# Kernel optimization log

Measured on AMD Instinct MI355X. Metric: run time of the kernel, lower is better.

Reference implementation:

```python
import jax, jax.numpy as jnp
import numpy as np

N_NODES = 100000
N_EDGES = 1600000
IN_CH = 128
OUT_CH = 64
NEG_SLOPE = 0.2
EPS = 1e-10


def setup_inputs() -> dict:
    key = jax.random.key(0)
    k1, k2, k3, k4, k5 = jax.random.split(key, 5)
    x = jax.random.normal(k1, (N_NODES, IN_CH), dtype=jnp.float32)
    edge_index = jax.random.randint(k2, (2, N_EDGES), 0, N_NODES, dtype=jnp.int64)
    W = jax.random.normal(k3, (OUT_CH, IN_CH), dtype=jnp.float32) * (1.0 / np.sqrt(IN_CH))
    a_l = jax.random.normal(k4, (OUT_CH,), dtype=jnp.float32) * (1.0 / np.sqrt(OUT_CH))
    a_r = jax.random.normal(k5, (OUT_CH,), dtype=jnp.float32) * (1.0 / np.sqrt(OUT_CH))
    bias = jnp.zeros((OUT_CH,), dtype=jnp.float32)
    return {"x": x, "edge_index": edge_index, "W": W, "a_l": a_l, "a_r": a_r, "bias": bias}


def reference(x, edge_index, W, a_l, a_r, bias):
    N = x.shape[0]
    h = x @ W.T                     # (N, out_ch)
    src, dst = edge_index[0], edge_index[1]
    e_l = h @ a_l                   # (N,)
    e_r = h @ a_r                   # (N,)
    edge_attn = jax.nn.leaky_relu(e_l[dst] + e_r[src], negative_slope=NEG_SLOPE)  # (E,)
    # segment softmax over incoming edges of each dst node
    edge_max = jax.ops.segment_max(edge_attn, dst, num_segments=N)  # (N,), -inf for isolated
    edge_attn = jnp.exp(edge_attn - edge_max[dst])
    edge_sum = jax.ops.segment_sum(edge_attn, dst, num_segments=N)  # (N,)
    edge_attn = edge_attn / (edge_sum[dst] + EPS)
    messages = h[src] * edge_attn[:, None]                          # (E, out_ch)
    out = jax.ops.segment_sum(messages, dst, num_segments=N)        # (N, out_ch)
    return out + bias
```

## Files before the change

### kernel.cpp

```cpp
#include <hip/hip_runtime.h>
#include <math.h>

#define NN 100000
#define NE 1600000
#define IC 128
#define OC 64
#define NEG_SLOPE 0.2f
#define EPS_F 1e-10f

#define NSLICE 500
#define SN 200
#define EB 500
#define QPB 800
#define CAP 3600
#define SLEN (NSLICE * EB)

typedef short bf16x8 __attribute__((ext_vector_type(8)));
typedef float f32x4 __attribute__((ext_vector_type(4)));

__device__ __forceinline__ unsigned short f2bf(float f) {
    unsigned u = __float_as_uint(f);
    u += 0x7fff + ((u >> 16) & 1);
    return (unsigned short)(u >> 16);
}

__global__ __launch_bounds__(256) void linear_kernel(
    const float* __restrict__ x, const float* __restrict__ W,
    const float* __restrict__ a_l, const float* __restrict__ a_r,
    unsigned short* __restrict__ h_bf, float* __restrict__ e_l,
    float* __restrict__ e_r)
{
    __shared__ unsigned short lds[128 * 136];
    const int tid = threadIdx.x;
    const int n0 = blockIdx.x * 64;

#pragma unroll
    for (int it = 0; it < 8; it++) {
        int i = it * 256 + tid;
        int r = i >> 5, c4 = i & 31;
        int n = n0 + r;
        float4 v = make_float4(0.f, 0.f, 0.f, 0.f);
        if (n < NN) v = *(const float4*)&x[(size_t)n * 128 + (c4 << 2)];
        ushort4 b;
        b.x = f2bf(v.x); b.y = f2bf(v.y); b.z = f2bf(v.z); b.w = f2bf(v.w);
        *(ushort4*)&lds[r * 136 + (c4 << 2)] = b;
    }
#pragma unroll
    for (int it = 0; it < 8; it++) {
        int i = it * 256 + tid;
        int r = i >> 5, c4 = i & 31;
        float4 v = *(const float4*)&W[r * 128 + (c4 << 2)];
        ushort4 b;
        b.x = f2bf(v.x); b.y = f2bf(v.y); b.z = f2bf(v.z); b.w = f2bf(v.w);
        *(ushort4*)&lds[(64 + r) * 136 + (c4 << 2)] = b;
    }
    __syncthreads();

    const int wv = tid >> 6;
    const int lane = tid & 63;
    const int q = lane >> 4;
    const int c = lane & 15;

    f32x4 acc[4];
#pragma unroll
    for (int t = 0; t < 4; t++) acc[t] = (f32x4){0.f, 0.f, 0.f, 0.f};

    const unsigned short* xrow = &lds[(wv * 16 + c) * 136];
    const unsigned short* wrow = &lds[(64 + c) * 136];

#pragma unroll
    for (int kk = 0; kk < 4; kk++) {
        int ko = kk * 32 + q * 8;
        bf16x8 a = *(const bf16x8*)&xrow[ko];
#pragma unroll
        for (int t = 0; t < 4; t++) {
            bf16x8 b = *(const bf16x8*)&wrow[t * 16 * 136 + ko];
            acc[t] = __builtin_amdgcn_mfma_f32_16x16x32_bf16(a, b, acc[t], 0, 0, 0);
        }
    }

#pragma unroll
    for (int r = 0; r < 4; r++) {
        int m = n0 + wv * 16 + q * 4 + r;
        if (m < NN) {
#pragma unroll
            for (int t = 0; t < 4; t++)
                h_bf[(size_t)m * OC + t * 16 + c] = f2bf(acc[t][r]);
        }
    }

    float al[4], ar[4];
#pragma unroll
    for (int t = 0; t < 4; t++) { al[t] = a_l[t * 16 + c]; ar[t] = a_r[t * 16 + c]; }
    float pl[4], pr[4];
#pragma unroll
    for (int r = 0; r < 4; r++) {
        pl[r] = al[0] * acc[0][r] + al[1] * acc[1][r] + al[2] * acc[2][r] + al[3] * acc[3][r];
        pr[r] = ar[0] * acc[0][r] + ar[1] * acc[1][r] + ar[2] * acc[2][r] + ar[3] * acc[3][r];
    }
#pragma unroll
    for (int m = 1; m < 16; m <<= 1) {
#pragma unroll
        for (int r = 0; r < 4; r++) {
            pl[r] += __shfl_xor(pl[r], m);
            pr[r] += __shfl_xor(pr[r], m);
        }
    }
    if (c == 0) {
#pragma unroll
        for (int r = 0; r < 4; r++) {
            int m = n0 + wv * 16 + q * 4 + r;
            if (m < NN) { e_l[m] = pl[r]; e_r[m] = pr[r]; }
        }
    }
}

__global__ __launch_bounds__(256) void hist_kernel(
    const int* __restrict__ dst, int* __restrict__ H)
{
    __shared__ int hist[NSLICE];
    const int t = threadIdx.x, b = blockIdx.x;
    for (int i = t; i < NSLICE; i += 256) hist[i] = 0;
    __syncthreads();
    for (int qi = t; qi < QPB; qi += 256) {
        int4 d = ((const int4*)dst)[b * QPB + qi];
        atomicAdd(&hist[d.x / SN], 1);
        atomicAdd(&hist[d.y / SN], 1);
        atomicAdd(&hist[d.z / SN], 1);
        atomicAdd(&hist[d.w / SN], 1);
    }
    __syncthreads();
    for (int i = t; i < NSLICE; i += 256) H[i * EB + b] = hist[i];
}

__global__ __launch_bounds__(1024) void scan_block_kernel(
    const int* __restrict__ deg, int* __restrict__ offsets,
    int* __restrict__ bsums)
{
    __shared__ int wsum[16];
    const int t = threadIdx.x;
    const int lane = t & 63, wv = t >> 6;
    const int i = blockIdx.x * 1024 + t;
    int v = (i < SLEN) ? deg[i] : 0;
    int incl = v;
#pragma unroll
    for (int off = 1; off < 64; off <<= 1) {
        int u = __shfl_up(incl, off);
        if (lane >= off) incl += u;
    }
    if (lane == 63) wsum[wv] = incl;
    __syncthreads();
    if (wv == 0 && lane < 16) {
        int s = wsum[lane];
        int si = s;
#pragma unroll
        for (int off = 1; off < 16; off <<= 1) {
            int u = __shfl_up(si, off);
            if (lane >= off) si += u;
        }
        wsum[lane] = si - s;
    }
    __syncthreads();
    int excl = incl - v + wsum[wv];
    if (i < SLEN) offsets[i] = excl;
    if (t == 1023) bsums[blockIdx.x] = excl + v;
}

__global__ __launch_bounds__(256) void scan_bsums_kernel(int* __restrict__ bsums)
{
    __shared__ int s[256];
    const int t = threadIdx.x;
    const int NB = (SLEN + 1023) / 1024;
    int v = (t < NB) ? bsums[t] : 0;
    s[t] = v;
    __syncthreads();
    for (int off = 1; off < 256; off <<= 1) {
        int u = (t >= off) ? s[t - off] : 0;
        __syncthreads();
        s[t] += u;
        __syncthreads();
    }
    if (t < NB) bsums[t] = s[t] - v;
}

__global__ __launch_bounds__(256) void bucket_kernel(
    const int* __restrict__ src, const int* __restrict__ dst,
    const int* __restrict__ O_raw, const int* __restrict__ bsums,
    int* __restrict__ bucketed)
{
    __shared__ int cur[NSLICE];
    const int t = threadIdx.x, b = blockIdx.x;
    for (int i = t; i < NSLICE; i += 256) {
        int gi = i * EB + b;
        cur[i] = O_raw[gi] + bsums[gi >> 10];
    }
    __syncthreads();
    for (int qi = t; qi < QPB; qi += 256) {
        int4 d4 = ((const int4*)dst)[b * QPB + qi];
        int4 s4 = ((const int4*)src)[b * QPB + qi];
        int dd[4] = {d4.x, d4.y, d4.z, d4.w};
        int ss[4] = {s4.x, s4.y, s4.z, s4.w};
#pragma unroll
        for (int k = 0; k < 4; k++) {
            int sl = dd[k] / SN;
            int pos = atomicAdd(&cur[sl], 1);
            bucketed[pos] = ((dd[k] - sl * SN) << 17) | ss[k];
        }
    }
}

__global__ __launch_bounds__(1024, 8) void fused_sort_agg_kernel(
    const int* __restrict__ bucketed, const int* __restrict__ O_raw,
    const int* __restrict__ bsums, const float* __restrict__ e_l,
    const float* __restrict__ e_r, const unsigned short* __restrict__ h_bf,
    const float* __restrict__ bias, float* __restrict__ out)
{
    __shared__ int2 sorted[CAP];
    __shared__ int hist[SN];
    __shared__ float el[SN];
    __shared__ int wsums[4];

    const int s = blockIdx.x, t = threadIdx.x;
    int gi0 = s * EB;
    const int B0 = O_raw[gi0] + bsums[gi0 >> 10];
    int B1 = NE;
    if (s < NSLICE - 1) {
        int gi1 = (s + 1) * EB;
        B1 = O_raw[gi1] + bsums[gi1 >> 10];
    }
    int cnt = B1 - B0;
    if (cnt > CAP) cnt = CAP;

    if (t < SN) {
        hist[t] = 0;
        el[t] = e_l[s * SN + t];
    }
    __syncthreads();

    int pr[4]; float wr[4];
#pragma unroll
    for (int k = 0; k < 4; k++) {
        int i = t + k * 1024;
        if (i < cnt) {
            int p = __builtin_nontemporal_load(&bucketed[B0 + i]);
            int dloc = p >> 17;
            float a = el[dloc] + e_r[p & 0x1FFFF];
            a = (a > 0.f) ? a : NEG_SLOPE * a;
            float w = __expf(a);
            pr[k] = p; wr[k] = w;
            atomicAdd(&hist[dloc], 1);
        }
    }
    __syncthreads();

    const int lane = t & 63, w4 = t >> 6;
    int v = (t < SN) ? hist[t] : 0;
    int incl = v;
#pragma unroll
    for (int o = 1; o < 64; o <<= 1) {
        int u = __shfl_up(incl, o);
        if (lane >= o) incl += u;
    }
    if (w4 < 4 && lane == 63) wsums[w4] = incl;
    __syncthreads();
    if (t == 0) {
        int run = 0;
#pragma unroll
        for (int k = 0; k < 4; k++) { int x = wsums[k]; wsums[k] = run; run += x; }
    }
    __syncthreads();
    int excl = incl - v + ((w4 < 4) ? wsums[w4] : 0);
    if (t < SN) hist[t] = excl;
    __syncthreads();

#pragma unroll
    for (int k = 0; k < 4; k++) {
        int i = t + k * 1024;
        if (i < cnt) {
            int dloc = pr[k] >> 17;
            int pos = atomicAdd(&hist[dloc], 1);
            sorted[pos] = make_int2(pr[k] & 0x1FFFF, __float_as_int(wr[k]));
        }
    }
    __syncthreads();

    const int g = t >> 3;
    const int ch = (t & 7) * 8;
    float4 bb0 = *(const float4*)&bias[ch];
    float4 bb1 = *(const float4*)&bias[ch + 4];

    for (int n = g; n < SN; n += 128) {
        const int start = (n == 0) ? 0 : hist[n - 1];
        const int end = hist[n];
        float acc[8] = {0.f, 0.f, 0.f, 0.f, 0.f, 0.f, 0.f, 0.f};
        float ws = 0.f;

        for (int j = start; j < end; j += 4) {
#pragma unroll
            for (int u = 0; u < 4; u++) {
                int e = j + u;
                int ec = (e < end) ? e : (end - 1);
                int2 p = sorted[ec];
                float w = (e < end) ? __int_as_float(p.y) : 0.f;
                const unsigned short* hp = h_bf + (((unsigned)p.x << 6) + ch);
                uint4 qv = *(const uint4*)hp;
                ws += w;
                acc[0] += w * __uint_as_float(qv.x << 16);
                acc[1] += w * __uint_as_float(qv.x & 0xffff0000u);
                acc[2] += w * __uint_as_float(qv.y << 16);
                acc[3] += w * __uint_as_float(qv.y & 0xffff0000u);
                acc[4] += w * __uint_as_float(qv.z << 16);
                acc[5] += w * __uint_as_float(qv.z & 0xffff0000u);
                acc[6] += w * __uint_as_float(qv.w << 16);
                acc[7] += w * __uint_as_float(qv.w & 0xffff0000u);
            }
        }

        float rinv = 1.0f / (ws + EPS_F);
        int node = s * SN + n;
        f32x4 o0 = { acc[0] * rinv + bb0.x, acc[1] * rinv + bb0.y,
                     acc[2] * rinv + bb0.z, acc[3] * rinv + bb0.w };
        f32x4 o1 = { acc[4] * rinv + bb1.x, acc[5] * rinv + bb1.y,
                     acc[6] * rinv + bb1.z, acc[7] * rinv + bb1.w };
        __builtin_nontemporal_store(o0, (f32x4*)&out[(size_t)node * OC + ch]);
        __builtin_nontemporal_store(o1, (f32x4*)&out[(size_t)node * OC + ch + 4]);
    }
}

extern "C" void kernel_launch(void* const* d_in, const int* in_sizes, int n_in,
                              void* d_out, int out_size, void* d_ws, size_t ws_size,
                              hipStream_t stream)
{
    const float* x = (const float*)d_in[0];
    const int* edge_index = (const int*)d_in[1];
    const float* W = (const float*)d_in[2];
    const float* a_l = (const float*)d_in[3];
    const float* a_r = (const float*)d_in[4];
    const float* bias = (const float*)d_in[5];
    float* out = (float*)d_out;

    const int* src = edge_index;
    const int* dst = edge_index + NE;

    char* w = (char*)d_ws;
    unsigned short* h_bf = (unsigned short*)w;
    size_t off = (size_t)NN * OC * 2;
    float* e_l = (float*)(w + off); off += (size_t)NN * 4;
    float* e_r = (float*)(w + off); off += (size_t)NN * 4;
    int* H = (int*)(w + off);       off += (size_t)SLEN * 4;
    int* O_raw = (int*)(w + off);   off += (size_t)(SLEN + 4) * 4;
    int* bsums = (int*)(w + off);   off += 256 * 4;
    int* bucketed = (int*)(w + off); off += (size_t)NE * 4;

    linear_kernel<<<(NN + 63) / 64, 256, 0, stream>>>(x, W, a_l, a_r, h_bf, e_l, e_r);
    hist_kernel<<<EB, 256, 0, stream>>>(dst, H);
    scan_block_kernel<<<(SLEN + 1023) / 1024, 1024, 0, stream>>>(H, O_raw, bsums);
    scan_bsums_kernel<<<1, 256, 0, stream>>>(bsums);
    bucket_kernel<<<EB, 256, 0, stream>>>(src, dst, O_raw, bsums, bucketed);
    fused_sort_agg_kernel<<<NSLICE, 1024, 0, stream>>>(bucketed, O_raw, bsums, e_l, e_r,
                                                       h_bf, bias, out);
}
```

Baseline: 175.4 us.

## Replace global scan-based bucketing with fixed-capacity slice segments and atomic cursors

```diff
diff --git a/kernel.cpp b/kernel.cpp
--- a/kernel.cpp
+++ b/kernel.cpp
@@ -12,8 +12,8 @@
 #define SN 200
 #define EB 500
 #define QPB 800
-#define CAP 3600
-#define SLEN (NSLICE * EB)
+#define EPB 3200
+#define CAPSEG 3600
 
 typedef short bf16x8 __attribute__((ext_vector_type(8)));
 typedef float f32x4 __attribute__((ext_vector_type(4)));
@@ -28,11 +28,15 @@
     const float* __restrict__ x, const float* __restrict__ W,
     const float* __restrict__ a_l, const float* __restrict__ a_r,
     unsigned short* __restrict__ h_bf, float* __restrict__ e_l,
-    float* __restrict__ e_r)
+    float* __restrict__ e_r, int* __restrict__ gcur)
 {
     __shared__ unsigned short lds[128 * 136];
     const int tid = threadIdx.x;
     const int n0 = blockIdx.x * 64;
+
+    if (blockIdx.x == 0) {
+        for (int i = tid; i < NSLICE; i += 256) gcur[i] = 0;
+    }
 
 #pragma unroll
     for (int it = 0; it < 8; it++) {
@@ -115,13 +119,21 @@
     }
 }
 
-__global__ __launch_bounds__(256) void hist_kernel(
-    const int* __restrict__ dst, int* __restrict__ H)
+__global__ __launch_bounds__(256) void bucket2_kernel(
+    const int* __restrict__ src, const int* __restrict__ dst,
+    int* __restrict__ gcur, int* __restrict__ bucketed)
 {
     __shared__ int hist[NSLICE];
+    __shared__ int base[NSLICE];
+    __shared__ int lcur[NSLICE];
+    __shared__ int gp[EPB];
+    __shared__ int pay[EPB];
+    __shared__ int wsums[4];
+
     const int t = threadIdx.x, b = blockIdx.x;
     for (int i = t; i < NSLICE; i += 256) hist[i] = 0;
     __syncthreads();
+
     for (int qi = t; qi < QPB; qi += 256) {
         int4 d = ((const int4*)dst)[b * QPB + qi];
         atomicAdd(&hist[d.x / SN], 1);
@@ -130,71 +142,40 @@
         atomicAdd(&hist[d.w / SN], 1);
     }
     __syncthreads();
-    for (int i = t; i < NSLICE; i += 256) H[i * EB + b] = hist[i];
-}
-
-__global__ __launch_bounds__(1024) void scan_block_kernel(
-    const int* __restrict__ deg, int* __restrict__ offsets,
-    int* __restrict__ bsums)
-{
-    __shared__ int wsum[16];
-    const int t = threadIdx.x;
-    const int lane = t & 63, wv = t >> 6;
-    const int i = blockIdx.x * 1024 + t;
-    int v = (i < SLEN) ? deg[i] : 0;
-    int incl = v;
-#pragma unroll
-    for (int off = 1; off < 64; off <<= 1) {
-        int u = __shfl_up(incl, off);
-        if (lane >= off) incl += u;
-    }
-    if (lane == 63) wsum[wv] = incl;
-    __syncthreads();
-    if (wv == 0 && lane < 16) {
-        int s = wsum[lane];
-        int si = s;
-#pragma unroll
-        for (int off = 1; off < 16; off <<= 1) {
-            int u = __shfl_up(si, off);
-            if (lane >= off) si += u;
-        }
-        wsum[lane] = si - s;
-    }
-    __syncthreads();
-    int excl = incl - v + wsum[wv];
-    if (i < SLEN) offsets[i] = excl;
-    if (t == 1023) bsums[blockIdx.x] = excl + v;
-}
-
-__global__ __launch_bounds__(256) void scan_bsums_kernel(int* __restrict__ bsums)
-{
-    __shared__ int s[256];
-    const int t = threadIdx.x;
-    const int NB = (SLEN + 1023) / 1024;
-    int v = (t < NB) ? bsums[t] : 0;
-    s[t] = v;
-    __syncthreads();
-    for (int off = 1; off < 256; off <<= 1) {
-        int u = (t >= off) ? s[t - off] : 0;
-        __syncthreads();
-        s[t] += u;
-        __syncthreads();
-    }
-    if (t < NB) bsums[t] = s[t] - v;
-}
-
-__global__ __launch_bounds__(256) void bucket_kernel(
-    const int* __restrict__ src, const int* __restrict__ dst,
-    const int* __restrict__ O_raw, const int* __restrict__ bsums,
-    int* __restrict__ bucketed)
-{
-    __shared__ int cur[NSLICE];
-    const int t = threadIdx.x, b = blockIdx.x;
-    for (int i = t; i < NSLICE; i += 256) {
-        int gi = i * EB + b;
-        cur[i] = O_raw[gi] + bsums[gi >> 10];
-    }
-    __syncthreads();
+
+    const int lane = t & 63, w4 = t >> 6;
+    int a0 = (2 * t < NSLICE) ? hist[2 * t] : 0;
+    int a1 = (2 * t + 1 < NSLICE) ? hist[2 * t + 1] : 0;
+    int pairsum = a0 + a1;
+    int incl = pairsum;
+#pragma unroll
+    for (int o = 1; o < 64; o <<= 1) {
+        int u = __shfl_up(incl, o);
+        if (lane >= o) incl += u;
+    }
+    if (lane == 63) wsums[w4] = incl;
+    __syncthreads();
+    if (t == 0) {
+        int run = 0;
+#pragma unroll
+        for (int k = 0; k < 4; k++) { int x = wsums[k]; wsums[k] = run; run += x; }
+    }
+    __syncthreads();
+    int excl = incl - pairsum + wsums[w4];
+    if (2 * t < NSLICE) {
+        int s0 = 2 * t;
+        base[s0] = s0 * CAPSEG + atomicAdd(&gcur[s0], a0);
+        hist[s0] = excl;
+        lcur[s0] = excl;
+    }
+    if (2 * t + 1 < NSLICE) {
+        int s1 = 2 * t + 1;
+        base[s1] = s1 * CAPSEG + atomicAdd(&gcur[s1], a1);
+        hist[s1] = excl + a0;
+        lcur[s1] = excl + a0;
+    }
+    __syncthreads();
+
     for (int qi = t; qi < QPB; qi += 256) {
         int4 d4 = ((const int4*)dst)[b * QPB + qi];
         int4 s4 = ((const int4*)src)[b * QPB + qi];
@@ -203,33 +184,36 @@
 #pragma unroll
         for (int k = 0; k < 4; k++) {
             int sl = dd[k] / SN;
-            int pos = atomicAdd(&cur[sl], 1);
-            bucketed[pos] = ((dd[k] - sl * SN) << 17) | ss[k];
-        }
+            int slot = atomicAdd(&lcur[sl], 1);
+            int gpos = base[sl] + (slot - hist[sl]);
+            if (gpos - sl * CAPSEG >= CAPSEG) gpos = -1;
+            gp[slot] = gpos;
+            pay[slot] = ((dd[k] - sl * SN) << 17) | ss[k];
+        }
+    }
+    __syncthreads();
+
+    for (int i = t; i < EPB; i += 256) {
+        int gpos = gp[i];
+        if (gpos >= 0) bucketed[gpos] = pay[i];
     }
 }
 
 __global__ __launch_bounds__(1024, 8) void fused_sort_agg_kernel(
-    const int* __restrict__ bucketed, const int* __restrict__ O_raw,
-    const int* __restrict__ bsums, const float* __restrict__ e_l,
-    const float* __restrict__ e_r, const unsigned short* __restrict__ h_bf,
-    const float* __restrict__ bias, float* __restrict__ out)
+    const int* __restrict__ bucketed, const int* __restrict__ gcur,
+    const float* __restrict__ e_l, const float* __restrict__ e_r,
+    const unsigned short* __restrict__ h_bf, const float* __restrict__ bias,
+    float* __restrict__ out)
 {
-    __shared__ int2 sorted[CAP];
+    __shared__ int2 sorted[CAPSEG];
     __shared__ int hist[SN];
     __shared__ float el[SN];
     __shared__ int wsums[4];
 
     const int s = blockIdx.x, t = threadIdx.x;
-    int gi0 = s * EB;
-    const int B0 = O_raw[gi0] + bsums[gi0 >> 10];
-    int B1 = NE;
-    if (s < NSLICE - 1) {
-        int gi1 = (s + 1) * EB;
-        B1 = O_raw[gi1] + bsums[gi1 >> 10];
-    }
-    int cnt = B1 - B0;
-    if (cnt > CAP) cnt = CAP;
+    const int B0 = s * CAPSEG;
+    int cnt = gcur[s];
+    if (cnt > CAPSEG) cnt = CAPSEG;
 
     if (t < SN) {
         hist[t] = 0;
@@ -296,23 +280,28 @@
         float ws = 0.f;
 
         for (int j = start; j < end; j += 4) {
+            int2 pp[4];
 #pragma unroll
             for (int u = 0; u < 4; u++) {
                 int e = j + u;
-                int ec = (e < end) ? e : (end - 1);
-                int2 p = sorted[ec];
-                float w = (e < end) ? __int_as_float(p.y) : 0.f;
-                const unsigned short* hp = h_bf + (((unsigned)p.x << 6) + ch);
-                uint4 qv = *(const uint4*)hp;
+                pp[u] = sorted[(e < end) ? e : (end - 1)];
+            }
+            uint4 qq[4];
+#pragma unroll
+            for (int u = 0; u < 4; u++)
+                qq[u] = *(const uint4*)(h_bf + (((unsigned)pp[u].x << 6) + ch));
+#pragma unroll
+            for (int u = 0; u < 4; u++) {
+                float w = (j + u < end) ? __int_as_float(pp[u].y) : 0.f;
                 ws += w;
-                acc[0] += w * __uint_as_float(qv.x << 16);
-                acc[1] += w * __uint_as_float(qv.x & 0xffff0000u);
-                acc[2] += w * __uint_as_float(qv.y << 16);
-                acc[3] += w * __uint_as_float(qv.y & 0xffff0000u);
-                acc[4] += w * __uint_as_float(qv.z << 16);
-                acc[5] += w * __uint_as_float(qv.z & 0xffff0000u);
-                acc[6] += w * __uint_as_float(qv.w << 16);
-                acc[7] += w * __uint_as_float(qv.w & 0xffff0000u);
+                acc[0] += w * __uint_as_float(qq[u].x << 16);
+                acc[1] += w * __uint_as_float(qq[u].x & 0xffff0000u);
+                acc[2] += w * __uint_as_float(qq[u].y << 16);
+                acc[3] += w * __uint_as_float(qq[u].y & 0xffff0000u);
+                acc[4] += w * __uint_as_float(qq[u].z << 16);
+                acc[5] += w * __uint_as_float(qq[u].z & 0xffff0000u);
+                acc[6] += w * __uint_as_float(qq[u].w << 16);
+                acc[7] += w * __uint_as_float(qq[u].w & 0xffff0000u);
             }
         }
 
@@ -347,16 +336,11 @@
     size_t off = (size_t)NN * OC * 2;
     float* e_l = (float*)(w + off); off += (size_t)NN * 4;
     float* e_r = (float*)(w + off); off += (size_t)NN * 4;
-    int* H = (int*)(w + off);       off += (size_t)SLEN * 4;
-    int* O_raw = (int*)(w + off);   off += (size_t)(SLEN + 4) * 4;
-    int* bsums = (int*)(w + off);   off += 256 * 4;
-    int* bucketed = (int*)(w + off); off += (size_t)NE * 4;
-
-    linear_kernel<<<(NN + 63) / 64, 256, 0, stream>>>(x, W, a_l, a_r, h_bf, e_l, e_r);
-    hist_kernel<<<EB, 256, 0, stream>>>(dst, H);
-    scan_block_kernel<<<(SLEN + 1023) / 1024, 1024, 0, stream>>>(H, O_raw, bsums);
-    scan_bsums_kernel<<<1, 256, 0, stream>>>(bsums);
-    bucket_kernel<<<EB, 256, 0, stream>>>(src, dst, O_raw, bsums, bucketed);
-    fused_sort_agg_kernel<<<NSLICE, 1024, 0, stream>>>(bucketed, O_raw, bsums, e_l, e_r,
+    int* gcur = (int*)(w + off);    off += (size_t)512 * 4;
+    int* bucketed = (int*)(w + off); off += (size_t)NSLICE * CAPSEG * 4;
+
+    linear_kernel<<<(NN + 63) / 64, 256, 0, stream>>>(x, W, a_l, a_r, h_bf, e_l, e_r, gcur);
+    bucket2_kernel<<<EB, 256, 0, stream>>>(src, dst, gcur, bucketed);
+    fused_sort_agg_kernel<<<NSLICE, 1024, 0, stream>>>(bucketed, gcur, e_l, e_r,
                                                        h_bf, bias, out);
 }
```

After: 174.5 us. Within noise of the previous version (-0.5%).
